# Kernel tuning notes

Hardware: AMD Instinct MI355X
Metric: run time of the kernel (lower is better)

## Reference

```python
import jax, jax.numpy as jnp
import numpy as np

HIDDEN = 768
NUM_BLOCKS = 8
BLOCK = HIDDEN // NUM_BLOCKS  # 96
FACTOR = 1
LAMBDA = 0.01  # sparsity_threshold
HTF = 1.0      # hard_thresholding_fraction
SCALE = 0.02


def setup_inputs() -> dict:
    key = jax.random.key(0)
    kx, k1, k2, k3, k4 = jax.random.split(key, 5)
    B, H, W = 2, 256, 256
    x = jax.random.normal(kx, (B, HIDDEN, H, W), dtype=jnp.float32)
    w1 = SCALE * jax.random.normal(k1, (NUM_BLOCKS, BLOCK, BLOCK * FACTOR, 2), dtype=jnp.float32)
    b1 = SCALE * jax.random.normal(k2, (NUM_BLOCKS, BLOCK * FACTOR, 1, 1, 2), dtype=jnp.float32)
    w2 = SCALE * jax.random.normal(k3, (NUM_BLOCKS, BLOCK * FACTOR, BLOCK, 2), dtype=jnp.float32)
    b2 = SCALE * jax.random.normal(k4, (NUM_BLOCKS, BLOCK, 1, 1, 2), dtype=jnp.float32)
    return {"x": x, "w1": w1, "b1": b1, "w2": w2, "b2": b2}


def _compl_mul_add(a, w, c):
    # a: (b,k,i,x,y,2) real/imag pairs; w: (k,i,o,2); c: (k,o,1,1,2)
    ar, ai = a[..., 0], a[..., 1]
    wr, wi = w[..., 0], w[..., 1]
    rr = jnp.einsum('bkixy,kio->bkoxy', ar, wr)
    ii = jnp.einsum('bkixy,kio->bkoxy', ai, wi)
    ir = jnp.einsum('bkixy,kio->bkoxy', ai, wr)
    ri = jnp.einsum('bkixy,kio->bkoxy', ar, wi)
    return jnp.stack([rr - ii, ir + ri], axis=-1) + c


def _softshrink(x, lam):
    return jnp.where(x > lam, x - lam, jnp.where(x < -lam, x + lam, jnp.zeros_like(x)))


def reference(x, w1, b1, w2, b2):
    B, C, H, W = x.shape
    total_modes = H // 2 + 1
    kept = int(total_modes * HTF)
    bias = x
    xf = jnp.fft.rfft2(x, s=(H, W), axes=(-2, -1), norm='ortho')  # (B,C,H,W//2+1)
    xf = xf.reshape(B, NUM_BLOCKS, BLOCK, H, W // 2 + 1)
    xr = jnp.stack([jnp.real(xf), jnp.imag(xf)], axis=-1)  # view_as_real
    lo, hi = total_modes - kept, total_modes + kept
    o1 = jax.nn.relu(_compl_mul_add(xr[:, :, :, lo:hi, :kept, :], w1, b1))
    o2 = jnp.zeros_like(xr).at[:, :, :, lo:hi, :kept, :].set(_compl_mul_add(o1, w2, b2))
    s = _softshrink(o2, LAMBDA)
    xc = (s[..., 0] + 1j * s[..., 1]).reshape(B, C, H, W // 2 + 1)
    out = jnp.fft.irfft2(xc, s=(H, W), axes=(-2, -1), norm='ortho').astype(x.dtype)
    return out + bias
```

## Files before the change

### kernel.cpp

```cpp
#include <hip/hip_runtime.h>
#include <hip/hip_bf16.h>
#include <math.h>


#define LAMBDA_SS 0.01f

typedef unsigned int u32;
typedef __attribute__((ext_vector_type(8))) short bf16x8;
typedef __attribute__((ext_vector_type(4))) float f32x4;

__device__ __forceinline__ u32 pack_bf16(float r, float i) {
  union { float f; u32 u; } ur, ui;
  ur.f = r; ui.f = i;
  u32 rb = (ur.u + 0x7FFFu + ((ur.u >> 16) & 1u)) >> 16;
  u32 ib = (ui.u + 0x7FFFu + ((ui.u >> 16) & 1u)) >> 16;
  return (ib << 16) | (rb & 0xFFFFu);
}

__device__ __forceinline__ float2 unpack_bf16(u32 p) {
  union { u32 u; float f; } a, b;
  a.u = (p & 0xFFFFu) << 16;
  b.u = (p & 0xFFFF0000u);
  return make_float2(a.f, b.f);
}

__device__ __forceinline__ float sshrink(float v) {
  return (v > LAMBDA_SS) ? v - LAMBDA_SS : ((v < -LAMBDA_SS) ? v + LAMBDA_SS : 0.f);
}

__device__ __forceinline__ float2 cadd(float2 a, float2 b){ return make_float2(a.x+b.x, a.y+b.y); }
__device__ __forceinline__ float2 csub(float2 a, float2 b){ return make_float2(a.x-b.x, a.y-b.y); }
__device__ __forceinline__ float2 cmul(float2 a, float2 b){
  return make_float2(fmaf(a.x,b.x,-a.y*b.y), fmaf(a.x,b.y,a.y*b.x));
}
__device__ __forceinline__ float2 cmulj(float2 a, float si){
  return make_float2(-si*a.y, si*a.x);
}
__device__ __forceinline__ float2 shflx(float2 v, int m){
  return make_float2(__shfl_xor(v.x, m, 64), __shfl_xor(v.y, m, 64));
}
__device__ __forceinline__ float2 shfll(float2 v, int l){
  return make_float2(__shfl(v.x, l, 64), __shfl(v.y, l, 64));
}
__device__ __forceinline__ int brev6(int x){ return (int)(__brev((u32)x) >> 26); }

struct Tw { float2 t128, t64, t32, t16, t8, t4; float si; };

__device__ __forceinline__ float2 mkTw(int e, float si){
  float a = (float)e * 0.0245436926f;
  return make_float2(cosf(a), si*sinf(a));
}
__device__ __forceinline__ Tw make_tw(int lane, float si){
  Tw w; w.si = si;
  w.t128 = mkTw(lane, si);
  w.t64  = mkTw(2*lane, si);
  w.t32  = mkTw((lane&31)*4, si);
  w.t16  = mkTw((lane&15)*8, si);
  w.t8   = mkTw((lane&7)*16, si);
  w.t4   = mkTw((lane&3)*32, si);
  return w;
}

__device__ __forceinline__ float2 bfly_dif(float2 v, int h, float2 th, int lane){
  float2 p = shflx(v, h);
  float sx = (lane & h) ? -1.f : 1.f;
  float2 s = make_float2(fmaf(sx, v.x, p.x), fmaf(sx, v.y, p.y));
  if (lane & h) s = cmul(s, th);
  return s;
}
__device__ __forceinline__ float2 bfly_dit(float2 v, int h, float2 th, int lane){
  if (lane & h) v = cmul(v, th);
  float2 p = shflx(v, h);
  float sx = (lane & h) ? -1.f : 1.f;
  return make_float2(fmaf(sx, v.x, p.x), fmaf(sx, v.y, p.y));
}

__device__ __forceinline__ void fft256_dif(float2 v[4], int lane, const Tw& T){
  float2 t128b = cmulj(T.t128, T.si);
  { float2 a=v[0], b=v[2]; v[0]=cadd(a,b); v[2]=cmul(csub(a,b), T.t128);
    float2 c=v[1], d=v[3]; v[1]=cadd(c,d); v[3]=cmul(csub(c,d), t128b); }
  { float2 a=v[0], b=v[1]; v[0]=cadd(a,b); v[1]=cmul(csub(a,b), T.t64);
    float2 c=v[2], d=v[3]; v[2]=cadd(c,d); v[3]=cmul(csub(c,d), T.t64); }
#pragma unroll
  for (int r=0;r<4;++r) v[r]=bfly_dif(v[r],32,T.t32,lane);
#pragma unroll
  for (int r=0;r<4;++r) v[r]=bfly_dif(v[r],16,T.t16,lane);
#pragma unroll
  for (int r=0;r<4;++r) v[r]=bfly_dif(v[r],8,T.t8,lane);
#pragma unroll
  for (int r=0;r<4;++r) v[r]=bfly_dif(v[r],4,T.t4,lane);
#pragma unroll
  for (int r=0;r<4;++r){
    float2 p=shflx(v[r],2);
    float sx=(lane&2)?-1.f:1.f;
    float2 s=make_float2(fmaf(sx,v[r].x,p.x), fmaf(sx,v[r].y,p.y));
    if ((lane&3)==3) s=cmulj(s,T.si);
    v[r]=s;
  }
#pragma unroll
  for (int r=0;r<4;++r){
    float2 p=shflx(v[r],1);
    float sx=(lane&1)?-1.f:1.f;
    v[r]=make_float2(fmaf(sx,v[r].x,p.x), fmaf(sx,v[r].y,p.y));
  }
}

__device__ __forceinline__ void fft256_dit(float2 v[4], int lane, const Tw& T){
#pragma unroll
  for (int r=0;r<4;++r){
    float2 p=shflx(v[r],1);
    float sx=(lane&1)?-1.f:1.f;
    v[r]=make_float2(fmaf(sx,v[r].x,p.x), fmaf(sx,v[r].y,p.y));
  }
#pragma unroll
  for (int r=0;r<4;++r){
    float2 w=v[r];
    if ((lane&3)==3) w=cmulj(w,T.si);
    float2 p=shflx(w,2);
    float sx=(lane&2)?-1.f:1.f;
    v[r]=make_float2(fmaf(sx,w.x,p.x), fmaf(sx,w.y,p.y));
  }
#pragma unroll
  for (int r=0;r<4;++r) v[r]=bfly_dit(v[r],4,T.t4,lane);
#pragma unroll
  for (int r=0;r<4;++r) v[r]=bfly_dit(v[r],8,T.t8,lane);
#pragma unroll
  for (int r=0;r<4;++r) v[r]=bfly_dit(v[r],16,T.t16,lane);
#pragma unroll
  for (int r=0;r<4;++r) v[r]=bfly_dit(v[r],32,T.t32,lane);
  { v[1]=cmul(v[1],T.t64); float2 a=v[0]; v[0]=cadd(a,v[1]); v[1]=csub(a,v[1]);
    v[3]=cmul(v[3],T.t64); float2 c=v[2]; v[2]=cadd(c,v[3]); v[3]=csub(c,v[3]); }
  { v[2]=cmul(v[2],T.t128); v[3]=cmul(v[3], cmulj(T.t128,T.si));
    float2 a=v[0]; v[0]=cadd(a,v[2]); v[2]=csub(a,v[2]);
    float2 b=v[1]; v[1]=cadd(b,v[3]); v[3]=csub(b,v[3]); }
}

__device__ __forceinline__ void make_tws4(int lane, float si, float2 tws[6][4]) {
#pragma unroll
  for (int r=0;r<4;++r){
    int e = (4*lane + r) & 127;
    float a = si * (float)e * 0.0245436926f;
    float sn, cs;
    sincosf(a, &sn, &cs);
    float2 t = make_float2(cs, sn);
    tws[0][r] = t;
#pragma unroll
    for (int s=1; s<6; ++s) {
      float2 sq = cmul(t, t);
      if (e & 64) { sq.x = -sq.x; sq.y = -sq.y; }
      e = (2*e) & 127;
      t = sq;
      tws[s][r] = t;
    }
  }
}

__device__ __forceinline__ void fft256_dif4(float2 v[4], int lane,
                                            const float2 tws[6][4], float si){
#pragma unroll
  for (int s=0;s<6;++s){
    const int m = 32>>s;
#pragma unroll
    for (int r=0;r<4;++r){
      float2 p = shflx(v[r], m);
      float sx = (lane & m) ? -1.f : 1.f;
      float2 t = make_float2(fmaf(sx, v[r].x, p.x), fmaf(sx, v[r].y, p.y));
      float2 tm = cmul(t, tws[s][r]);
      v[r] = (lane & m) ? tm : t;
    }
  }
  { float2 a0=v[0], a2=v[2]; v[0]=cadd(a0,a2); v[2]=csub(a0,a2);
    float2 a1=v[1], a3=v[3]; v[1]=cadd(a1,a3); v[3]=cmulj(csub(a1,a3), si); }
  { float2 a=v[0]; v[0]=cadd(a,v[1]); v[1]=csub(a,v[1]);
    float2 c=v[2]; v[2]=cadd(c,v[3]); v[3]=csub(c,v[3]); }
}

__device__ __forceinline__ void fft256_dit4(float2 v[4], int lane,
                                            const float2 tws[6][4], float si){
  { float2 a=v[0]; v[0]=cadd(a,v[1]); v[1]=csub(a,v[1]);
    float2 c=v[2]; v[2]=cadd(c,v[3]); v[3]=csub(c,v[3]); }
  { v[3] = cmulj(v[3], si);
    float2 a0=v[0]; v[0]=cadd(a0,v[2]); v[2]=csub(a0,v[2]);
    float2 a1=v[1]; v[1]=cadd(a1,v[3]); v[3]=csub(a1,v[3]); }
#pragma unroll
  for (int s=5;s>=0;--s){
    const int m = 32>>s;
#pragma unroll
    for (int r=0;r<4;++r){
      float2 wm_ = cmul(v[r], tws[s][r]);
      float2 w = (lane & m) ? wm_ : v[r];
      float2 p = shflx(w, m);
      float sx = (lane & m) ? -1.f : 1.f;
      v[r] = make_float2(fmaf(sx, w.x, p.x), fmaf(sx, w.y, p.y));
    }
  }
}

__device__ __forceinline__ int stage_row(int kw){ return 33*(kw&3) + (kw>>2); }
__device__ __forceinline__ int dslot(int n){ return (((n>>2)&7) ^ ((n&3)<<1)) << 4; }

__global__ __launch_bounds__(256) void k_rowfft(const float* __restrict__ x, u32* __restrict__ F) {
  __shared__ u32 stage[131*65];
  const int bc = blockIdx.x >> 2, hc = blockIdx.x & 3;
  const int tid = threadIdx.x, wave = tid >> 6, lane = tid & 63;
  Tw T = make_tw(lane, -1.f);
  const int L = brev6(lane);
  const int laneP0 = brev6((64 - L) & 63);
  const int lanePX = 63 - lane;

  for (int rr = 0; rr < 8; ++rr) {
    const int hl0 = wave*16 + rr*2, hl1 = hl0 + 1;
    const float* xa = x + ((size_t)bc*256 + hc*64 + hl0) * 256;
    float2 v[4];
#pragma unroll
    for (int r=0;r<4;++r){ int d = lane + 64*r; v[r] = make_float2(xa[d], xa[256+d]); }
    fft256_dif(v, lane, T);
#define UNSCR(R, RP, C, LP) { \
      float2 z = v[R]; float2 p = shfll(v[RP], LP); \
      float2 A  = make_float2(0.5f*(z.x+p.x), 0.5f*(z.y-p.y)); \
      float2 Bv = make_float2(0.5f*(z.y+p.y), 0.5f*(p.x-z.x)); \
      int kw = 4*L + (C); \
      if (kw <= 128) { int row = stage_row(kw); \
        stage[row*65 + hl0] = pack_bf16(A.x, A.y); \
        stage[row*65 + hl1] = pack_bf16(Bv.x, Bv.y); } }
    UNSCR(0, 0, 0, laneP0)
    UNSCR(1, 1, 2, lanePX)
    UNSCR(2, 3, 1, lanePX)
    UNSCR(3, 2, 3, lanePX)
#undef UNSCR
  }
  __syncthreads();
  for (int idx = tid; idx < 129*64; idx += 256) {
    int kw = idx >> 6, hl = idx & 63;
    F[((size_t)bc*129 + kw)*256 + hc*64 + hl] = stage[stage_row(kw)*65 + hl];
  }
}

__global__ __launch_bounds__(256) void k_prep_w(const float2* __restrict__ w1,
                                                const float2* __restrict__ w2,
                                                u32* __restrict__ Wt) {
  const int blk = blockIdx.x;
  const int k = blk >> 1, layer = blk & 1;
  const float2* w = (layer == 0 ? w1 : w2) + (size_t)k * 96 * 96;
  u32* out = Wt + (size_t)blk * 18432;
  for (int idx = threadIdx.x; idx < 9216; idx += 256) {
    int o = idx % 96, i = idx / 96;
    float2 v = w[i * 96 + o];
    out[(2 * o) * 96 + i]     = pack_bf16(v.x, -v.y);
    out[(2 * o + 1) * 96 + i] = pack_bf16(v.y, v.x);
  }
}

#define CM_LDS_BYTES 99072

__global__ __launch_bounds__(1024) void k_colmix(u32* __restrict__ F,
    const u32* __restrict__ Wt,
    const float2* __restrict__ b1, const float2* __restrict__ b2) {
  extern __shared__ char smem[];

  const int bi = (blockIdx.x & 7) * 258 + (blockIdx.x >> 3);
  const int kw = bi % 129;
  const int bk = bi / 129;
  const int k = bk & 7, b = bk >> 3;
  const int t = threadIdx.x;
  const int lane = t & 63, wave = t >> 6;
  const int wm = wave >> 2, wn = wave & 3;
  const int lrow = lane & 15;
  const int g = lane >> 4;

  const size_t chstride = 129 * 256;
  const size_t colbase = (((size_t)(b*768 + k*96)) * 129 + kw) * 256;

  {
    uint4 raw[6];
#pragma unroll
    for (int cc = 0; cc < 6; ++cc)
      raw[cc] = *reinterpret_cast<const uint4*>(F + colbase + (size_t)(wave*6 + cc)*chstride + 4*lane);

    float2 tws[6][4];
    make_tws4(lane, -1.f, tws);
    const float s = 1.f/256.f;
#pragma unroll
    for (int pp = 0; pp < 3; ++pp) {
      float2 va[4], vb[4];
      va[0]=unpack_bf16(raw[2*pp].x);   va[1]=unpack_bf16(raw[2*pp].y);
      va[2]=unpack_bf16(raw[2*pp].z);   va[3]=unpack_bf16(raw[2*pp].w);
      vb[0]=unpack_bf16(raw[2*pp+1].x); vb[1]=unpack_bf16(raw[2*pp+1].y);
      vb[2]=unpack_bf16(raw[2*pp+1].z); vb[3]=unpack_bf16(raw[2*pp+1].w);
      fft256_dif4(va, lane, tws, -1.f);
      fft256_dif4(vb, lane, tws, -1.f);
      const int c0 = wave*6 + 2*pp;
#pragma unroll
      for (int r = 0; r < 4; ++r) {
        int n = 4*lane + r;
        int byte = (n*384 + c0*4) ^ dslot(n);
        *reinterpret_cast<uint2*>(smem + byte) =
            make_uint2(pack_bf16(va[r].x*s, va[r].y*s), pack_bf16(vb[r].x*s, vb[r].y*s));
      }
    }
  }
  __syncthreads();

  const bf16x8* W1v = reinterpret_cast<const bf16x8*>(Wt + (size_t)(k*2 + 0) * 18432);
  const bf16x8* W2v = reinterpret_cast<const bf16x8*>(Wt + (size_t)(k*2 + 1) * 18432);

  f32x4 acc[3][4];

#pragma unroll
  for (int mi = 0; mi < 3; ++mi)
#pragma unroll
    for (int ni = 0; ni < 4; ++ni) acc[mi][ni] = (f32x4)0.f;
  {
#pragma unroll
    for (int ks = 0; ks < 6; ++ks) {
      bf16x8 bf[4];
#pragma unroll
      for (int ni = 0; ni < 4; ++ni) {
        int n = wn*64 + ni*16 + lrow;
        int byte = (n*384 + ks*64 + g*16) ^ dslot(n);
        bf[ni] = *reinterpret_cast<bf16x8*>(smem + byte);
      }
      bf16x8 af[3];
#pragma unroll
      for (int mi = 0; mi < 3; ++mi)
        af[mi] = W1v[(wm*48 + mi*16 + lrow)*24 + ks*4 + g];
#pragma unroll
      for (int ni = 0; ni < 4; ++ni)
#pragma unroll
        for (int mi = 0; mi < 3; ++mi)
          acc[mi][ni] = __builtin_amdgcn_mfma_f32_16x16x32_bf16(af[mi], bf[ni], acc[mi][ni], 0, 0, 0);
    }
  }
  __syncthreads();

  {
    const float2* b1k = b1 + k * 96;
#pragma unroll
    for (int mi = 0; mi < 3; ++mi) {
      int m0 = wm*48 + mi*16 + 4*g;
      int o0 = m0 >> 1;
      float2 ba = b1k[o0], bb = b1k[o0 + 1];
#pragma unroll
      for (int ni = 0; ni < 4; ++ni) {
        int n = wn*64 + ni*16 + lrow;
        f32x4 v = acc[mi][ni];
        u32 lo = pack_bf16(fmaxf(v[0] + ba.x, 0.f), fmaxf(v[1] + ba.y, 0.f));
        u32 hi = pack_bf16(fmaxf(v[2] + bb.x, 0.f), fmaxf(v[3] + bb.y, 0.f));
        int byte = (n*384 + m0*2) ^ dslot(n);
        *reinterpret_cast<uint2*>(smem + byte) = make_uint2(lo, hi);
      }
    }
  }
  __syncthreads();

#pragma unroll
  for (int mi = 0; mi < 3; ++mi)
#pragma unroll
    for (int ni = 0; ni < 4; ++ni) acc[mi][ni] = (f32x4)0.f;
  {
#pragma unroll
    for (int ks = 0; ks < 6; ++ks) {
      bf16x8 bf[4];
#pragma unroll
      for (int ni = 0; ni < 4; ++ni) {
        int n = wn*64 + ni*16 + lrow;
        int byte = (n*384 + ks*64 + g*16) ^ dslot(n);
        bf[ni] = *reinterpret_cast<bf16x8*>(smem + byte);
      }
      bf16x8 af[3];
#pragma unroll
      for (int mi = 0; mi < 3; ++mi)
        af[mi] = W2v[(wm*48 + mi*16 + lrow)*24 + ks*4 + g];
#pragma unroll
      for (int ni = 0; ni < 4; ++ni)
#pragma unroll
        for (int mi = 0; mi < 3; ++mi)
          acc[mi][ni] = __builtin_amdgcn_mfma_f32_16x16x32_bf16(af[mi], bf[ni], acc[mi][ni], 0, 0, 0);
    }
  }
  __syncthreads();

  {
    u32* Clds = reinterpret_cast<u32*>(smem);
    const float2* b2k = b2 + k * 96;
#pragma unroll
    for (int mi = 0; mi < 3; ++mi) {
      int m0 = wm*48 + mi*16 + 4*g;
      int o0 = m0 >> 1;
      float2 ca = b2k[o0], cb = b2k[o0 + 1];
#pragma unroll
      for (int ni = 0; ni < 4; ++ni) {
        int n = wn*64 + ni*16 + lrow;
        f32x4 v = acc[mi][ni];
        Clds[o0*258 + n]       = pack_bf16(sshrink(v[0] + ca.x), sshrink(v[1] + ca.y));
        Clds[(o0 + 1)*258 + n] = pack_bf16(sshrink(v[2] + cb.x), sshrink(v[3] + cb.y));
      }
    }
  }
  __syncthreads();

  {
    const u32* Clds = reinterpret_cast<const u32*>(smem);
    float2 tws[6][4];
    make_tws4(lane, 1.f, tws);
    const float s = 1.f/256.f;
#pragma unroll
    for (int pp = 0; pp < 3; ++pp) {
      const int c0 = wave*6 + 2*pp;
      float2 va[4], vb[4];
      {
        uint2 q0 = *reinterpret_cast<const uint2*>(Clds + c0*258 + 4*lane);
        uint2 q1 = *reinterpret_cast<const uint2*>(Clds + c0*258 + 4*lane + 2);
        va[0]=unpack_bf16(q0.x); va[1]=unpack_bf16(q0.y);
        va[2]=unpack_bf16(q1.x); va[3]=unpack_bf16(q1.y);
        uint2 q2 = *reinterpret_cast<const uint2*>(Clds + (c0+1)*258 + 4*lane);
        uint2 q3 = *reinterpret_cast<const uint2*>(Clds + (c0+1)*258 + 4*lane + 2);
        vb[0]=unpack_bf16(q2.x); vb[1]=unpack_bf16(q2.y);
        vb[2]=unpack_bf16(q3.x); vb[3]=unpack_bf16(q3.y);
      }
      fft256_dit4(va, lane, tws, 1.f);
      fft256_dit4(vb, lane, tws, 1.f);
      uint4 oa, ob;
      oa.x = pack_bf16(va[0].x*s, va[0].y*s); oa.y = pack_bf16(va[1].x*s, va[1].y*s);
      oa.z = pack_bf16(va[2].x*s, va[2].y*s); oa.w = pack_bf16(va[3].x*s, va[3].y*s);
      ob.x = pack_bf16(vb[0].x*s, vb[0].y*s); ob.y = pack_bf16(vb[1].x*s, vb[1].y*s);
      ob.z = pack_bf16(vb[2].x*s, vb[2].y*s); ob.w = pack_bf16(vb[3].x*s, vb[3].y*s);
      *reinterpret_cast<uint4*>(F + colbase + (size_t)c0*chstride + 4*lane) = oa;
      *reinterpret_cast<uint4*>(F + colbase + (size_t)(c0+1)*chstride + 4*lane) = ob;
    }
  }
}

__global__ __launch_bounds__(256) void k_rowifft(const u32* __restrict__ F,
                                                 const float* __restrict__ x,
                                                 float* __restrict__ out) {
  __shared__ u32 stage[131*65];
  const int bc = blockIdx.x >> 2, hc = blockIdx.x & 3;
  const int tid = threadIdx.x, wave = tid >> 6, lane = tid & 63;
  Tw T = make_tw(lane, 1.f);
  for (int idx = tid; idx < 129*64; idx += 256) {
    int kw = idx >> 6, hl = idx & 63;
    stage[stage_row(kw)*65 + hl] = F[((size_t)bc*129 + kw)*256 + hc*64 + hl];
  }
  __syncthreads();

  const int L = brev6(lane);
  for (int rr = 0; rr < 8; ++rr) {
    const int hl0 = wave*16 + rr*2, hl1 = hl0 + 1;
    float2 v[4];
#pragma unroll
    for (int r=0;r<4;++r) {
      int c = ((r&1)<<1) | (r>>1);
      int kw = 4*L + c;
      int src = (kw <= 128) ? kw : 256 - kw;
      float sg = (kw <= 128) ? 1.f : -1.f;
      int row = stage_row(src);
      float2 a = unpack_bf16(stage[row*65 + hl0]);
      float2 b = unpack_bf16(stage[row*65 + hl1]);
      a.y *= sg; b.y *= sg;
      if (kw == 0 || kw == 128) { a.y = 0.f; b.y = 0.f; }
      v[r] = make_float2(a.x - b.y, a.y + b.x);
    }
    fft256_dit(v, lane, T);
    const float* xa = x   + ((size_t)bc*256 + hc*64 + hl0) * 256;
    float*       oa = out + ((size_t)bc*256 + hc*64 + hl0) * 256;
#pragma unroll
    for (int r=0;r<4;++r) {
      int d = lane + 64*r;
      oa[d]       = v[r].x + xa[d];
      oa[256 + d] = v[r].y + xa[256 + d];
    }
  }
}

extern "C" void kernel_launch(void* const* d_in, const int* in_sizes, int n_in,
                              void* d_out, int out_size, void* d_ws, size_t ws_size,
                              hipStream_t stream) {
  const float* x   = (const float*)d_in[0];
  const float2* w1 = (const float2*)d_in[1];
  const float2* b1 = (const float2*)d_in[2];
  const float2* w2 = (const float2*)d_in[3];
  const float2* b2 = (const float2*)d_in[4];
  float* out = (float*)d_out;
  u32* F = (u32*)d_ws;
  u32* Wt = (u32*)d_out;

  (void)hipFuncSetAttribute(reinterpret_cast<const void*>(k_colmix),
                            hipFuncAttributeMaxDynamicSharedMemorySize, CM_LDS_BYTES);

  const int n_rows_blocks = 1536 * 4;
  const int n_cm_blocks   = 2 * 8 * 129;

  k_prep_w<<<16, 256, 0, stream>>>(w1, w2, Wt);
  k_rowfft<<<n_rows_blocks, 256, 0, stream>>>(x, F);
  k_colmix<<<n_cm_blocks, 1024, CM_LDS_BYTES, stream>>>(F, Wt, b1, b2);
  k_rowifft<<<n_rows_blocks, 256, 0, stream>>>(F, x, out);
}
```

Baseline: 880.4 us.

## Halve colmix workgroup to 512 threads with doubled per-wave work

The column-mix kernel now launches 512 threads instead of 1024. Each wave handles 12 channels in the column FFT stages and a 96-row M tile (6 MFMA row tiles) in the two complex GEMMs. The aim is more work per wave, better reuse of each weight fragment across N tiles, and wider 16-byte LDS writes. The cost is that with 8 waves instead of 16, per-wave register pressure rises from 24 accumulators and the 4-column FFT batches. Because LDS use is unchanged at about 99 KB, only one block may fit per CU despite the launch_bounds(512,2) hint, which could lower latency hiding.

Measured after the change: 932.8 us. +6.0%, slower.

```diff
diff --git a/kernel.cpp b/kernel.cpp
--- a/kernel.cpp
+++ b/kernel.cpp
@@ -253,7 +253,7 @@
 
 #define CM_LDS_BYTES 99072
 
-__global__ __launch_bounds__(1024) void k_colmix(u32* __restrict__ F,
+__global__ __launch_bounds__(512, 2) void k_colmix(u32* __restrict__ F,
     const u32* __restrict__ Wt,
     const float2* __restrict__ b1, const float2* __restrict__ b2) {
   extern __shared__ char smem[];
@@ -272,30 +272,31 @@
   const size_t colbase = (((size_t)(b*768 + k*96)) * 129 + kw) * 256;
 
   {
-    uint4 raw[6];
-#pragma unroll
-    for (int cc = 0; cc < 6; ++cc)
-      raw[cc] = *reinterpret_cast<const uint4*>(F + colbase + (size_t)(wave*6 + cc)*chstride + 4*lane);
-
     float2 tws[6][4];
     make_tws4(lane, -1.f, tws);
     const float s = 1.f/256.f;
 #pragma unroll
-    for (int pp = 0; pp < 3; ++pp) {
-      float2 va[4], vb[4];
-      va[0]=unpack_bf16(raw[2*pp].x);   va[1]=unpack_bf16(raw[2*pp].y);
-      va[2]=unpack_bf16(raw[2*pp].z);   va[3]=unpack_bf16(raw[2*pp].w);
-      vb[0]=unpack_bf16(raw[2*pp+1].x); vb[1]=unpack_bf16(raw[2*pp+1].y);
-      vb[2]=unpack_bf16(raw[2*pp+1].z); vb[3]=unpack_bf16(raw[2*pp+1].w);
-      fft256_dif4(va, lane, tws, -1.f);
-      fft256_dif4(vb, lane, tws, -1.f);
-      const int c0 = wave*6 + 2*pp;
+    for (int bt = 0; bt < 3; ++bt) {
+      const int c0 = wave*12 + bt*4;
+      float2 v4[4][4];
+#pragma unroll
+      for (int cc = 0; cc < 4; ++cc) {
+        uint4 raw = *reinterpret_cast<const uint4*>(F + colbase + (size_t)(c0+cc)*chstride + 4*lane);
+        v4[cc][0]=unpack_bf16(raw.x); v4[cc][1]=unpack_bf16(raw.y);
+        v4[cc][2]=unpack_bf16(raw.z); v4[cc][3]=unpack_bf16(raw.w);
+      }
+#pragma unroll
+      for (int cc = 0; cc < 4; ++cc) fft256_dif4(v4[cc], lane, tws, -1.f);
 #pragma unroll
       for (int r = 0; r < 4; ++r) {
         int n = 4*lane + r;
         int byte = (n*384 + c0*4) ^ dslot(n);
-        *reinterpret_cast<uint2*>(smem + byte) =
-            make_uint2(pack_bf16(va[r].x*s, va[r].y*s), pack_bf16(vb[r].x*s, vb[r].y*s));
+        uint4 w;
+        w.x = pack_bf16(v4[0][r].x*s, v4[0][r].y*s);
+        w.y = pack_bf16(v4[1][r].x*s, v4[1][r].y*s);
+        w.z = pack_bf16(v4[2][r].x*s, v4[2][r].y*s);
+        w.w = pack_bf16(v4[3][r].x*s, v4[3][r].y*s);
+        *reinterpret_cast<uint4*>(smem + byte) = w;
       }
     }
   }
@@ -304,31 +305,23 @@
   const bf16x8* W1v = reinterpret_cast<const bf16x8*>(Wt + (size_t)(k*2 + 0) * 18432);
   const bf16x8* W2v = reinterpret_cast<const bf16x8*>(Wt + (size_t)(k*2 + 1) * 18432);
 
-  f32x4 acc[3][4];
-
-#pragma unroll
-  for (int mi = 0; mi < 3; ++mi)
+  f32x4 acc[6][4];
+
+#pragma unroll
+  for (int mi = 0; mi < 6; ++mi)
 #pragma unroll
     for (int ni = 0; ni < 4; ++ni) acc[mi][ni] = (f32x4)0.f;
-  {
-#pragma unroll
-    for (int ks = 0; ks < 6; ++ks) {
-      bf16x8 bf[4];
+#pragma unroll
+  for (int ks = 0; ks < 6; ++ks) {
+#pragma unroll
+    for (int mi = 0; mi < 6; ++mi) {
+      bf16x8 af = W1v[(wm*96 + mi*16 + lrow)*24 + ks*4 + g];
 #pragma unroll
       for (int ni = 0; ni < 4; ++ni) {
         int n = wn*64 + ni*16 + lrow;
-        int byte = (n*384 + ks*64 + g*16) ^ dslot(n);
-        bf[ni] = *reinterpret_cast<bf16x8*>(smem + byte);
-      }
-      bf16x8 af[3];
-#pragma unroll
-      for (int mi = 0; mi < 3; ++mi)
-        af[mi] = W1v[(wm*48 + mi*16 + lrow)*24 + ks*4 + g];
-#pragma unroll
-      for (int ni = 0; ni < 4; ++ni)
-#pragma unroll
-        for (int mi = 0; mi < 3; ++mi)
-          acc[mi][ni] = __builtin_amdgcn_mfma_f32_16x16x32_bf16(af[mi], bf[ni], acc[mi][ni], 0, 0, 0);
+        bf16x8 bf = *reinterpret_cast<bf16x8*>(smem + ((n*384 + ks*64 + g*16) ^ dslot(n)));
+        acc[mi][ni] = __builtin_amdgcn_mfma_f32_16x16x32_bf16(af, bf, acc[mi][ni], 0, 0, 0);
+      }
     }
   }
   __syncthreads();
@@ -336,8 +329,8 @@
   {
     const float2* b1k = b1 + k * 96;
 #pragma unroll
-    for (int mi = 0; mi < 3; ++mi) {
-      int m0 = wm*48 + mi*16 + 4*g;
+    for (int mi = 0; mi < 6; ++mi) {
+      int m0 = wm*96 + mi*16 + 4*g;
       int o0 = m0 >> 1;
       float2 ba = b1k[o0], bb = b1k[o0 + 1];
 #pragma unroll
@@ -354,28 +347,20 @@
   __syncthreads();
 
 #pragma unroll
-  for (int mi = 0; mi < 3; ++mi)
+  for (int mi = 0; mi < 6; ++mi)
 #pragma unroll
     for (int ni = 0; ni < 4; ++ni) acc[mi][ni] = (f32x4)0.f;
-  {
-#pragma unroll
-    for (int ks = 0; ks < 6; ++ks) {
-      bf16x8 bf[4];
+#pragma unroll
+  for (int ks = 0; ks < 6; ++ks) {
+#pragma unroll
+    for (int mi = 0; mi < 6; ++mi) {
+      bf16x8 af = W2v[(wm*96 + mi*16 + lrow)*24 + ks*4 + g];
 #pragma unroll
       for (int ni = 0; ni < 4; ++ni) {
         int n = wn*64 + ni*16 + lrow;
-        int byte = (n*384 + ks*64 + g*16) ^ dslot(n);
-        bf[ni] = *reinterpret_cast<bf16x8*>(smem + byte);
-      }
-      bf16x8 af[3];
-#pragma unroll
-      for (int mi = 0; mi < 3; ++mi)
-        af[mi] = W2v[(wm*48 + mi*16 + lrow)*24 + ks*4 + g];
-#pragma unroll
-      for (int ni = 0; ni < 4; ++ni)
-#pragma unroll
-        for (int mi = 0; mi < 3; ++mi)
-          acc[mi][ni] = __builtin_amdgcn_mfma_f32_16x16x32_bf16(af[mi], bf[ni], acc[mi][ni], 0, 0, 0);
+        bf16x8 bf = *reinterpret_cast<bf16x8*>(smem + ((n*384 + ks*64 + g*16) ^ dslot(n)));
+        acc[mi][ni] = __builtin_amdgcn_mfma_f32_16x16x32_bf16(af, bf, acc[mi][ni], 0, 0, 0);
+      }
     }
   }
   __syncthreads();
@@ -384,8 +369,8 @@
     u32* Clds = reinterpret_cast<u32*>(smem);
     const float2* b2k = b2 + k * 96;
 #pragma unroll
-    for (int mi = 0; mi < 3; ++mi) {
-      int m0 = wm*48 + mi*16 + 4*g;
+    for (int mi = 0; mi < 6; ++mi) {
+      int m0 = wm*96 + mi*16 + 4*g;
       int o0 = m0 >> 1;
       float2 ca = b2k[o0], cb = b2k[o0 + 1];
 #pragma unroll
@@ -405,28 +390,27 @@
     make_tws4(lane, 1.f, tws);
     const float s = 1.f/256.f;
 #pragma unroll
-    for (int pp = 0; pp < 3; ++pp) {
-      const int c0 = wave*6 + 2*pp;
-      float2 va[4], vb[4];
-      {
-        uint2 q0 = *reinterpret_cast<const uint2*>(Clds + c0*258 + 4*lane);
-        uint2 q1 = *reinterpret_cast<const uint2*>(Clds + c0*258 + 4*lane + 2);
-        va[0]=unpack_bf16(q0.x); va[1]=unpack_bf16(q0.y);
-        va[2]=unpack_bf16(q1.x); va[3]=unpack_bf16(q1.y);
-        uint2 q2 = *reinterpret_cast<const uint2*>(Clds + (c0+1)*258 + 4*lane);
-        uint2 q3 = *reinterpret_cast<const uint2*>(Clds + (c0+1)*258 + 4*lane + 2);
-        vb[0]=unpack_bf16(q2.x); vb[1]=unpack_bf16(q2.y);
-        vb[2]=unpack_bf16(q3.x); vb[3]=unpack_bf16(q3.y);
-      }
-      fft256_dit4(va, lane, tws, 1.f);
-      fft256_dit4(vb, lane, tws, 1.f);
-      uint4 oa, ob;
-      oa.x = pack_bf16(va[0].x*s, va[0].y*s); oa.y = pack_bf16(va[1].x*s, va[1].y*s);
-      oa.z = pack_bf16(va[2].x*s, va[2].y*s); oa.w = pack_bf16(va[3].x*s, va[3].y*s);
-      ob.x = pack_bf16(vb[0].x*s, vb[0].y*s); ob.y = pack_bf16(vb[1].x*s, vb[1].y*s);
-      ob.z = pack_bf16(vb[2].x*s, vb[2].y*s); ob.w = pack_bf16(vb[3].x*s, vb[3].y*s);
-      *reinterpret_cast<uint4*>(F + colbase + (size_t)c0*chstride + 4*lane) = oa;
-      *reinterpret_cast<uint4*>(F + colbase + (size_t)(c0+1)*chstride + 4*lane) = ob;
+    for (int bt = 0; bt < 3; ++bt) {
+      const int c0 = wave*12 + bt*4;
+      float2 v4[4][4];
+#pragma unroll
+      for (int cc = 0; cc < 4; ++cc) {
+        uint2 q0 = *reinterpret_cast<const uint2*>(Clds + (c0+cc)*258 + 4*lane);
+        uint2 q1 = *reinterpret_cast<const uint2*>(Clds + (c0+cc)*258 + 4*lane + 2);
+        v4[cc][0]=unpack_bf16(q0.x); v4[cc][1]=unpack_bf16(q0.y);
+        v4[cc][2]=unpack_bf16(q1.x); v4[cc][3]=unpack_bf16(q1.y);
+      }
+#pragma unroll
+      for (int cc = 0; cc < 4; ++cc) fft256_dit4(v4[cc], lane, tws, 1.f);
+#pragma unroll
+      for (int cc = 0; cc < 4; ++cc) {
+        uint4 o;
+        o.x = pack_bf16(v4[cc][0].x*s, v4[cc][0].y*s);
+        o.y = pack_bf16(v4[cc][1].x*s, v4[cc][1].y*s);
+        o.z = pack_bf16(v4[cc][2].x*s, v4[cc][2].y*s);
+        o.w = pack_bf16(v4[cc][3].x*s, v4[cc][3].y*s);
+        *reinterpret_cast<uint4*>(F + colbase + (size_t)(c0+cc)*chstride + 4*lane) = o;
+      }
     }
   }
 }
@@ -493,6 +477,6 @@
 
   k_prep_w<<<16, 256, 0, stream>>>(w1, w2, Wt);
   k_rowfft<<<n_rows_blocks, 256, 0, stream>>>(x, F);
-  k_colmix<<<n_cm_blocks, 1024, CM_LDS_BYTES, stream>>>(F, Wt, b1, b2);
+  k_colmix<<<n_cm_blocks, 512, CM_LDS_BYTES, stream>>>(F, Wt, b1, b2);
   k_rowifft<<<n_rows_blocks, 256, 0, stream>>>(F, x, out);
 }
```
